# Optimization experiments

Measured on AMD Instinct MI355X. Metric: run time of the kernel, lower is better.

The kernel has to match this reference:

```python
import jax, jax.numpy as jnp
import numpy as np

ALPHA = 0.2  # LeakyReLU negative slope (init alpha)


def setup_inputs() -> dict:
    key = jax.random.key(0)
    k1, k2, k3, k4 = jax.random.split(key, 4)
    B, N, D = 32, 1024, 64
    H, E = 4, 16  # n_heads, out_features per head
    return {
        "input": jax.random.normal(k1, (B, N, D), dtype=jnp.float32),
        "adj": jax.random.uniform(k2, (N, N), dtype=jnp.float32),  # unused by the module
        "W": jax.random.normal(k3, (H, D, E), dtype=jnp.float32) * 0.1,
        "a": jax.random.normal(k4, (2 * E, 1), dtype=jnp.float32) * 0.1,
    }


def reference(input, adj, W, a):
    # h: [B, H, N, E]
    h = jnp.einsum('bnd,hde->bhne', input, W)
    E = h.shape[-1]
    # Original concatenates [h_j, h_i] along features then dots with a,
    # i.e. e[b,h,i,j] = leakyrelu(a[:E]\cdot h_j + a[E:]\cdot h_i).
    a_dst = a[:E, 0]   # applied to the softmax (j) axis
    a_src = a[E:, 0]   # applied to the query (i) axis
    s_src = jnp.einsum('bhne,e->bhn', h, a_src)  # [B,H,N]
    s_dst = jnp.einsum('bhne,e->bhn', h, a_dst)  # [B,H,N]
    e = jax.nn.leaky_relu(s_src[..., :, None] + s_dst[..., None, :],
                          negative_slope=ALPHA)  # [B,H,N,N]
    attention = jax.nn.softmax(e, axis=-1)  # dropout skipped (eval mode)
    h_prime = jnp.einsum('bhij,bhje->bhie', attention, h)  # [B,H,N,E]
    B, H, N, _ = h_prime.shape
    # Faithful to torch: .view(B, N, -1) on a [B,H,N,E] contiguous tensor
    # is a raw row-major reshape (no transpose), reproduced exactly here.
    return h_prime.reshape(B, N, H * E)
```

## Files before the change

### kernel.cpp

```cpp
#include <hip/hip_runtime.h>

typedef _Float16 f16;
typedef f16 f16x8 __attribute__((ext_vector_type(8)));
typedef float f32x4 __attribute__((ext_vector_type(4)));

constexpr int Bc = 32, Nc = 1024, Dc = 64, Hc = 4, Ec = 16;
constexpr int HP = 1032;

__global__ __launch_bounds__(256) void gat_proj(const float* __restrict__ input,
                                                const float* __restrict__ W,
                                                const float* __restrict__ a,
                                                f16* __restrict__ h16t,
                                                float* __restrict__ s_src,
                                                float* __restrict__ s_dst) {
    __shared__ float W_lds[Dc * Ec];
    __shared__ float a_lds[2 * Ec];

    const int tid = threadIdx.x;
    const int gid = blockIdx.x * 256 + tid;
    const int n   = gid & (Nc - 1);
    const int bh  = gid >> 10;
    const int hh  = bh & (Hc - 1);
    const int b   = bh >> 2;

    ((float4*)W_lds)[tid] = ((const float4*)(W + hh * Dc * Ec))[tid];
    if (tid < 2 * Ec) a_lds[tid] = a[tid];
    __syncthreads();

    const float4* in_row = (const float4*)(input + ((size_t)b * Nc + n) * Dc);

    float acc[Ec];
#pragma unroll
    for (int e = 0; e < Ec; ++e) acc[e] = 0.f;

#pragma unroll
    for (int d4 = 0; d4 < Dc / 4; ++d4) {
        float4 x = in_row[d4];
        float xs[4] = {x.x, x.y, x.z, x.w};
#pragma unroll
        for (int k = 0; k < 4; ++k) {
            const float xv = xs[k];
            const float* wrow = &W_lds[(d4 * 4 + k) * Ec];
#pragma unroll
            for (int e = 0; e < Ec; ++e) acc[e] = fmaf(xv, wrow[e], acc[e]);
        }
    }

    f16* hb = h16t + (size_t)bh * Ec * HP + n;
#pragma unroll
    for (int e = 0; e < Ec; ++e) hb[e * HP] = (f16)acc[e];

    float sd = 0.f, ss = 0.f;
#pragma unroll
    for (int e = 0; e < Ec; ++e) {
        sd = fmaf(acc[e], a_lds[e], sd);
        ss = fmaf(acc[e], a_lds[Ec + e], ss);
    }
    s_dst[gid] = sd;
    s_src[gid] = ss;
}

__global__ __launch_bounds__(512) void gat_attn5(const f16* __restrict__ h16t,
                                                 const float* __restrict__ s_src,
                                                 const float* __restrict__ s_dst,
                                                 float* __restrict__ out) {
    __shared__ alignas(16) f16 h_t[Ec * HP];
    __shared__ alignas(16) f16 u_lds[Nc];
    __shared__ alignas(16) f16 v_lds[Nc];
    __shared__ float red[8];

    const int bh    = blockIdx.x;
    const int ihalf = blockIdx.y;
    const int tid   = threadIdx.x;
    const int lane  = tid & 63;
    const int wave  = tid >> 6;
    const int row   = lane & 15;
    const int quad  = lane >> 4;

    {
        const float4* src = (const float4*)(h16t + (size_t)bh * Ec * HP);
        float4* dst = (float4*)h_t;
        dst[tid]        = src[tid];
        dst[512 + tid]  = src[512 + tid];
        dst[1024 + tid] = src[1024 + tid];
        dst[1536 + tid] = src[1536 + tid];
        if (tid < 16) dst[2048 + tid] = src[2048 + tid];
    }

    const float sd0 = s_dst[bh * Nc + tid];
    const float sd1 = s_dst[bh * Nc + 512 + tid];
    {
        float m = fmaxf(sd0, sd1);
#pragma unroll
        for (int off = 1; off < 64; off <<= 1) m = fmaxf(m, __shfl_xor(m, off, 64));
        if (lane == 0) red[wave] = m;
    }
    __syncthreads();
    float maxd = red[0];
#pragma unroll
    for (int w = 1; w < 8; ++w) maxd = fmaxf(maxd, red[w]);

    u_lds[tid]       = (f16)__expf(sd0 - maxd);
    u_lds[512 + tid] = (f16)__expf(sd1 - maxd);
    v_lds[tid]       = (f16)__expf(0.2f * (sd0 - maxd));
    v_lds[512 + tid] = (f16)__expf(0.2f * (sd1 - maxd));

    const int ibase = ihalf * 512 + wave * 64;
    f16x8 C8[4];
#pragma unroll
    for (int it = 0; it < 4; ++it) {
        const float si = s_src[bh * Nc + ibase + it * 16 + row];
        const float c1 = si + maxd;
        const float Cf = (c1 >= 0.f) ? __expf(-0.8f * c1) : 1.0f;
        const f16 ch = (f16)Cf;
        C8[it] = (f16x8){ch, ch, ch, ch, ch, ch, ch, ch};
    }
    __syncthreads();

    f32x4 accN[4] = {};
    f32x4 accD[4] = {};
    const f16 o1 = (f16)1.f;
    const f16x8 ones = {o1, o1, o1, o1, o1, o1, o1, o1};

    const f16* up = u_lds + quad * 8;
    const f16* vp = v_lds + quad * 8;
    const f16* bp = h_t + row * HP + quad * 8;

#pragma unroll 4
    for (int kt = 0; kt < 32; ++kt) {
        const f16x8 u8 = *(const f16x8*)(up + kt * 32);
        const f16x8 v8 = *(const f16x8*)(vp + kt * 32);
        const f16x8 b8 = *(const f16x8*)(bp + kt * 32);
#pragma unroll
        for (int it = 0; it < 4; ++it) {
            const f16x8 p = __builtin_elementwise_max(u8, C8[it] * v8);
            accN[it] = __builtin_amdgcn_mfma_f32_16x16x32_f16(p, b8,   accN[it], 0, 0, 0);
            accD[it] = __builtin_amdgcn_mfma_f32_16x16x32_f16(p, ones, accD[it], 0, 0, 0);
        }
    }

#pragma unroll
    for (int it = 0; it < 4; ++it) {
#pragma unroll
        for (int r = 0; r < 4; ++r) {
            const float inv = __builtin_amdgcn_rcpf(accD[it][r]);
            const int i = ibase + it * 16 + quad * 4 + r;
            out[((size_t)(bh * Nc + i)) * Ec + row] = accN[it][r] * inv;
        }
    }
}

extern "C" void kernel_launch(void* const* d_in, const int* in_sizes, int n_in,
                              void* d_out, int out_size, void* d_ws, size_t ws_size,
                              hipStream_t stream) {
    const float* input = (const float*)d_in[0];
    const float* W = (const float*)d_in[2];
    const float* a = (const float*)d_in[3];
    float* out = (float*)d_out;

    char* ws = (char*)d_ws;
    f16*   h16t  = (f16*)(ws);
    float* s_src = (float*)(ws + 4227072);
    float* s_dst = (float*)(ws + 4227072 + 524288);

    gat_proj<<<dim3(Bc * Hc * Nc / 256), dim3(256), 0, stream>>>(input, W, a, h16t,
                                                                 s_src, s_dst);
    gat_attn5<<<dim3(Bc * Hc, 2), dim3(512), 0, stream>>>(h16t, s_src, s_dst, out);
}
```

Measured before the change: 26.66 us.

## Fuse projection into attention kernel with MFMA projection and folded W·a scores

Drops the separate projection kernel and its workspace round-trip. Each attention block now computes its own h tile in LDS using f16 MFMA over the input rows, and computes the source/destination scores directly from the input with W·a vectors folded in LDS. This removes one launch and the global write/read of h and the scores. In exchange each of the two i-half blocks redundantly recomputes the full projection and rereads the input. It also adds f16 rounding of the inputs before projection.

```diff
diff --git a/kernel.cpp b/kernel.cpp
--- a/kernel.cpp
+++ b/kernel.cpp
@@ -1,96 +1,97 @@
 #include <hip/hip_runtime.h>
 
 typedef _Float16 f16;
+typedef f16 f16x4 __attribute__((ext_vector_type(4)));
 typedef f16 f16x8 __attribute__((ext_vector_type(8)));
 typedef float f32x4 __attribute__((ext_vector_type(4)));
 
 constexpr int Bc = 32, Nc = 1024, Dc = 64, Hc = 4, Ec = 16;
-constexpr int HP = 1032;
+constexpr int HPL = 1032;
 
-__global__ __launch_bounds__(256) void gat_proj(const float* __restrict__ input,
-                                                const float* __restrict__ W,
-                                                const float* __restrict__ a,
-                                                f16* __restrict__ h16t,
-                                                float* __restrict__ s_src,
-                                                float* __restrict__ s_dst) {
-    __shared__ float W_lds[Dc * Ec];
-    __shared__ float a_lds[2 * Ec];
-
-    const int tid = threadIdx.x;
-    const int gid = blockIdx.x * 256 + tid;
-    const int n   = gid & (Nc - 1);
-    const int bh  = gid >> 10;
-    const int hh  = bh & (Hc - 1);
-    const int b   = bh >> 2;
-
-    ((float4*)W_lds)[tid] = ((const float4*)(W + hh * Dc * Ec))[tid];
-    if (tid < 2 * Ec) a_lds[tid] = a[tid];
-    __syncthreads();
-
-    const float4* in_row = (const float4*)(input + ((size_t)b * Nc + n) * Dc);
-
-    float acc[Ec];
-#pragma unroll
-    for (int e = 0; e < Ec; ++e) acc[e] = 0.f;
-
-#pragma unroll
-    for (int d4 = 0; d4 < Dc / 4; ++d4) {
-        float4 x = in_row[d4];
-        float xs[4] = {x.x, x.y, x.z, x.w};
-#pragma unroll
-        for (int k = 0; k < 4; ++k) {
-            const float xv = xs[k];
-            const float* wrow = &W_lds[(d4 * 4 + k) * Ec];
-#pragma unroll
-            for (int e = 0; e < Ec; ++e) acc[e] = fmaf(xv, wrow[e], acc[e]);
-        }
-    }
-
-    f16* hb = h16t + (size_t)bh * Ec * HP + n;
-#pragma unroll
-    for (int e = 0; e < Ec; ++e) hb[e * HP] = (f16)acc[e];
-
-    float sd = 0.f, ss = 0.f;
-#pragma unroll
-    for (int e = 0; e < Ec; ++e) {
-        sd = fmaf(acc[e], a_lds[e], sd);
-        ss = fmaf(acc[e], a_lds[Ec + e], ss);
-    }
-    s_dst[gid] = sd;
-    s_src[gid] = ss;
-}
-
-__global__ __launch_bounds__(512) void gat_attn5(const f16* __restrict__ h16t,
-                                                 const float* __restrict__ s_src,
-                                                 const float* __restrict__ s_dst,
+__global__ __launch_bounds__(512) void gat_fused(const float* __restrict__ input,
+                                                 const float* __restrict__ W,
+                                                 const float* __restrict__ a,
                                                  float* __restrict__ out) {
-    __shared__ alignas(16) f16 h_t[Ec * HP];
+    __shared__ alignas(16) f16 h_t[Ec * HPL];
+    __shared__ alignas(16) float wa_lds[2][Dc];
+    __shared__ float ss_lds[Nc];
     __shared__ alignas(16) f16 u_lds[Nc];
     __shared__ alignas(16) f16 v_lds[Nc];
     __shared__ float red[8];
 
     const int bh    = blockIdx.x;
     const int ihalf = blockIdx.y;
+    const int hh    = bh & (Hc - 1);
+    const int b     = bh >> 2;
     const int tid   = threadIdx.x;
     const int lane  = tid & 63;
     const int wave  = tid >> 6;
     const int row   = lane & 15;
     const int quad  = lane >> 4;
 
-    {
-        const float4* src = (const float4*)(h16t + (size_t)bh * Ec * HP);
-        float4* dst = (float4*)h_t;
-        dst[tid]        = src[tid];
-        dst[512 + tid]  = src[512 + tid];
-        dst[1024 + tid] = src[1024 + tid];
-        dst[1536 + tid] = src[1536 + tid];
-        if (tid < 16) dst[2048 + tid] = src[2048 + tid];
+    if (tid < Dc) {
+        const float* wr = W + hh * Dc * Ec + tid * Ec;
+        float wd = 0.f, wsx = 0.f;
+#pragma unroll
+        for (int e = 0; e < Ec; ++e) {
+            wd  = fmaf(wr[e], a[e],      wd);
+            wsx = fmaf(wr[e], a[Ec + e], wsx);
+        }
+        wa_lds[0][tid] = wd;
+        wa_lds[1][tid] = wsx;
     }
 
-    const float sd0 = s_dst[bh * Nc + tid];
-    const float sd1 = s_dst[bh * Nc + 512 + tid];
+    f16x8 bW0, bW1;
     {
-        float m = fmaxf(sd0, sd1);
+        const float* wp = W + hh * Dc * Ec + row;
+#pragma unroll
+        for (int j = 0; j < 8; ++j) {
+            bW0[j] = (f16)wp[(quad * 8 + j) * Ec];
+            bW1[j] = (f16)wp[(32 + quad * 8 + j) * Ec];
+        }
+    }
+
+#pragma unroll
+    for (int t = 0; t < 8; ++t) {
+        const int n0 = wave * 128 + t * 16;
+        const float* ip = input + ((size_t)b * Nc + n0 + row) * Dc;
+        f16x8 x0, x1;
+#pragma unroll
+        for (int j = 0; j < 8; ++j) {
+            x0[j] = (f16)ip[quad * 8 + j];
+            x1[j] = (f16)ip[32 + quad * 8 + j];
+        }
+        f32x4 hD = {};
+        hD = __builtin_amdgcn_mfma_f32_16x16x32_f16(x0, bW0, hD, 0, 0, 0);
+        hD = __builtin_amdgcn_mfma_f32_16x16x32_f16(x1, bW1, hD, 0, 0, 0);
+        f16x4 hp;
+#pragma unroll
+        for (int r = 0; r < 4; ++r) hp[r] = (f16)hD[r];
+        *(f16x4*)(&h_t[row * HPL + n0 + quad * 4]) = hp;
+    }
+    __syncthreads();
+
+    float sdv[2], ssv[2];
+#pragma unroll
+    for (int nn = 0; nn < 2; ++nn) {
+        const int n = nn * 512 + tid;
+        const float4* xr  = (const float4*)(input + ((size_t)b * Nc + n) * Dc);
+        const float4* wdp = (const float4*)wa_lds[0];
+        const float4* wsp = (const float4*)wa_lds[1];
+        float sd = 0.f, ss = 0.f;
+#pragma unroll
+        for (int d4 = 0; d4 < 16; ++d4) {
+            float4 x = xr[d4], wd = wdp[d4], wsx = wsp[d4];
+            sd = fmaf(x.x, wd.x,  fmaf(x.y, wd.y,  fmaf(x.z, wd.z,  fmaf(x.w, wd.w,  sd))));
+            ss = fmaf(x.x, wsx.x, fmaf(x.y, wsx.y, fmaf(x.z, wsx.z, fmaf(x.w, wsx.w, ss))));
+        }
+        sdv[nn] = sd;
+        ssv[nn] = ss;
+        ss_lds[n] = ss;
+    }
+
+    {
+        float m = fmaxf(sdv[0], sdv[1]);
 #pragma unroll
         for (int off = 1; off < 64; off <<= 1) m = fmaxf(m, __shfl_xor(m, off, 64));
         if (lane == 0) red[wave] = m;
@@ -100,16 +101,16 @@
 #pragma unroll
     for (int w = 1; w < 8; ++w) maxd = fmaxf(maxd, red[w]);
 
-    u_lds[tid]       = (f16)__expf(sd0 - maxd);
-    u_lds[512 + tid] = (f16)__expf(sd1 - maxd);
-    v_lds[tid]       = (f16)__expf(0.2f * (sd0 - maxd));
-    v_lds[512 + tid] = (f16)__expf(0.2f * (sd1 - maxd));
+    u_lds[tid]       = (f16)__expf(sdv[0] - maxd);
+    u_lds[512 + tid] = (f16)__expf(sdv[1] - maxd);
+    v_lds[tid]       = (f16)__expf(0.2f * (sdv[0] - maxd));
+    v_lds[512 + tid] = (f16)__expf(0.2f * (sdv[1] - maxd));
 
     const int ibase = ihalf * 512 + wave * 64;
     f16x8 C8[4];
 #pragma unroll
     for (int it = 0; it < 4; ++it) {
-        const float si = s_src[bh * Nc + ibase + it * 16 + row];
+        const float si = ss_lds[ibase + it * 16 + row];
         const float c1 = si + maxd;
         const float Cf = (c1 >= 0.f) ? __expf(-0.8f * c1) : 1.0f;
         const f16 ch = (f16)Cf;
@@ -124,7 +125,7 @@
 
     const f16* up = u_lds + quad * 8;
     const f16* vp = v_lds + quad * 8;
-    const f16* bp = h_t + row * HP + quad * 8;
+    const f16* bp = h_t + row * HPL + quad * 8;
 
 #pragma unroll 4
     for (int kt = 0; kt < 32; ++kt) {
@@ -158,12 +159,5 @@
     const float* a = (const float*)d_in[3];
     float* out = (float*)d_out;
 
-    char* ws = (char*)d_ws;
-    f16*   h16t  = (f16*)(ws);
-    float* s_src = (float*)(ws + 4227072);
-    float* s_dst = (float*)(ws + 4227072 + 524288);
-
-    gat_proj<<<dim3(Bc * Hc * Nc / 256), dim3(256), 0, stream>>>(input, W, a, h16t,
-                                                                 s_src, s_dst);
-    gat_attn5<<<dim3(Bc * Hc, 2), dim3(512), 0, stream>>>(h16t, s_src, s_dst, out);
+    gat_fused<<<dim3(Bc * Hc, 2), dim3(512), 0, stream>>>(input, W, a, out);
 }
```

After: 36.95 us. 1.39x slower.
